# Performance work log

Hardware: AMD Instinct MI355X
Metric: run time of the kernel (lower is better)

The kernel has to match this reference:

```python
import jax, jax.numpy as jnp
import numpy as np

# ---- forest structure (static) ----
B = 32                      # number of trees in the batch
DEPTH = 12                  # topological levels per tree
LEVELS = [2 ** d for d in range(DEPTH)]           # nodes per level (root=level 0)
STARTS = np.concatenate([[0], np.cumsum(LEVELS)[:-1]]).astype(int)
NPG = int(sum(LEVELS))      # 4095 nodes per graph, node 0 = root
N = B * NPG                 # 131040 total nodes
VOCAB = 20000               # dataset.PAD_TOKEN_VALUE + 1
PAD = VOCAB - 1             # padding_idx
E = 256                     # embedding_dim (x_size)
H = 256                     # lstm_output_dim (h_size)
C = 104                     # num_classes (extra_non_linear=None)


def setup_inputs() -> dict:
    key = jax.random.key(0)
    ks = jax.random.split(key, 8)
    # random parent in the previous level for every non-root node (irregular fan-in)
    rng = np.random.RandomState(0)
    par = np.full(N, -1, dtype=np.int64)
    for g in range(B):
        off = g * NPG
        for d in range(1, DEPTH):
            nd = LEVELS[d]
            par[off + STARTS[d]: off + STARTS[d] + nd] = (
                off + STARTS[d - 1] + rng.randint(0, LEVELS[d - 1], size=nd))
    s = 0.05
    return {
        'x': jax.random.randint(ks[0], (N,), 0, VOCAB),
        'par': jnp.asarray(par),
        'emb': jax.random.normal(ks[1], (VOCAB, E), jnp.float32) * s,
        'W_iou': jax.random.normal(ks[2], (3 * H, E), jnp.float32) * s,
        'U_iou': jax.random.normal(ks[3], (3 * H, H), jnp.float32) * s,
        'b_iou': jnp.zeros((1, 3 * H), jnp.float32),
        'U_f_w': jax.random.normal(ks[4], (H, H), jnp.float32) * s,
        'U_f_b': jnp.zeros((H,), jnp.float32),
        'lin_w': jax.random.normal(ks[5], (C, H), jnp.float32) * s,
        'lin_b': jnp.zeros((C,), jnp.float32),
    }


def _forward(x, par, emb, W_iou, U_iou, b_iou, U_f_w, U_f_b, lin_w, lin_b):
    emb = emb.at[PAD].set(0.0)                 # padding_idx row is zero
    x_vec = emb[x]                             # [N, E]
    iou = x_vec @ W_iou.T                      # [N, 3H], W_iou has no bias
    h = jnp.zeros((N, H), x_vec.dtype)
    c = jnp.zeros((N, H), x_vec.dtype)
    offs = jnp.arange(B) * NPG
    # topological propagation: leaves (deepest level) -> root, per generation
    for d in range(DEPTH - 1, -1, -1):
        nd = LEVELS[d]
        nids = (offs[:, None] + STARTS[d] + jnp.arange(nd)).reshape(-1)  # [B*nd]
        iou_n = iou[nids]
        if d < DEPTH - 1:
            nc = LEVELS[d + 1]
            cids = (offs[:, None] + STARTS[d + 1] + jnp.arange(nc)).reshape(-1)
            h_ch = h[cids]                     # mailbox gather of child states
            c_ch = c[cids]
            p = par[cids]                      # global parent id per child
            seg = (p // NPG) * nd + (p % NPG - STARTS[d])  # parent slot in this level
            f = jax.nn.sigmoid(h_ch @ U_f_w.T + U_f_b)     # per-child forget gate
            h_tild = jax.ops.segment_sum(h_ch, seg, num_segments=B * nd)
            c_agg = jax.ops.segment_sum(f * c_ch, seg, num_segments=B * nd)
            iou_n = iou_n + h_tild @ U_iou.T
            c_n = c_agg
        else:
            c_n = jnp.zeros((B * nd, H), x_vec.dtype)
        iou_n = iou_n + b_iou
        i, o, u = jnp.split(iou_n, 3, axis=1)
        c_new = jax.nn.sigmoid(i) * jnp.tanh(u) + c_n
        h_new = jax.nn.sigmoid(o) * jnp.tanh(c_new)
        h = h.at[nids].set(h_new)
        c = c.at[nids].set(c_new)
    roots = h[offs]                            # graph.ndata['h'][0] per graph
    return roots @ lin_w.T + lin_b             # [B, num_classes]


def reference(x, par, emb, W_iou, U_iou, b_iou, U_f_w, U_f_b, lin_w, lin_b):
    return _forward(x, par, emb, W_iou, U_iou, b_iou, U_f_w, U_f_b, lin_w, lin_b)
```

## Files before the change

### kernel.cpp

```cpp
#include <hip/hip_runtime.h>
#include <hip/hip_bf16.h>


#define B_G     32
#define NPG     4095
#define NTOT    (B_G * NPG)
#define NCLS    104
#define VOCAB   20000
#define PAD_TOK 19999
#define KCAP    24
#define LB(d)   (32 * ((1 << (d)) - 1))

#define EMB_BLKS  2500
#define WUC_BLKS  1536
#define UFC_BLKS  256
#define PREP_BLKS 512
#define CONV_BLKS (EMB_BLKS + WUC_BLKS + UFC_BLKS + PREP_BLKS)

typedef unsigned short u16;
typedef unsigned int   u32;
typedef __attribute__((ext_vector_type(8))) short bfrag8;
typedef __attribute__((ext_vector_type(4))) float ffrag4;

__device__ __forceinline__ float bf2f(u16 v) {
    union { u32 u; float f; } x; x.u = ((u32)v) << 16; return x.f;
}
__device__ __forceinline__ u16 f2bf(float f) {
    union { __hip_bfloat16 h; u16 u; } c; c.h = __float2bfloat16(f); return c.u;
}
__device__ __forceinline__ float loadv(const void* b, int i, int isf32) {
    return isf32 ? ((const float*)b)[i] : bf2f(((const u16*)b)[i]);
}
__device__ __forceinline__ float sigf(float x) { return 1.f / (1.f + __expf(-x)); }

__device__ __forceinline__ void gll16(const u16* g, u16* l) {
    __builtin_amdgcn_global_load_lds(
        (const __attribute__((address_space(1))) u32*)g,
        (__attribute__((address_space(3))) u32*)l, 16, 0, 0);
}

__global__ __launch_bounds__(384) void probe_kernel(
    const void* emb, const void* Wiou, const void* Uiou,
    const void* Ufw, const void* lw,
    const int* x32, const int* par32, int* flags)
{
    if (blockIdx.x != 0) return;
    const int w = threadIdx.x >> 6, lane = threadIdx.x & 63;
    const void* ptrs[5] = { emb, Wiou, Uiou, Ufw, lw };
    if (w < 5) {
        const u16* p = (const u16*)ptrs[w];
        int big = 0;
        #pragma unroll
        for (int k = 0; k < 2; ++k) {
            u32 e = (((u32)p[lane * 2 + k]) << 16 >> 23) & 0xFF;
            if (e >= 129) ++big;
        }
        unsigned long long m1 = __ballot(big >= 1);
        unsigned long long m2 = __ballot(big >= 2);
        int tot = __popcll(m1) + __popcll(m2);
        if (lane == 0) flags[w] = (tot >= 4) ? 1 : 0;
    } else if (w == 5) {
        int bad = (lane < 8) ? (x32[2 * lane + 1] != 0) : 0;
        unsigned long long mx = __ballot(bad != 0);
        if (lane == 0) {
            flags[5] = (mx == 0) ? 1 : 0;
            flags[6] = (par32[3] == 0 && par32[5] == 0) ? 1 : 0;
        }
    }
}

__global__ __launch_bounds__(256) void convert_kernel(
    const void* __restrict__ emb, u16* __restrict__ embb,
    const void* __restrict__ Wiou, const void* __restrict__ Uiou,
    u16* __restrict__ wuc,
    const void* __restrict__ Ufw, u16* __restrict__ ufc,
    const int* __restrict__ x, const int* __restrict__ par,
    int* __restrict__ tokLvl, int* __restrict__ cnt, int* __restrict__ bucket,
    const int* __restrict__ flags)
{
    const int b = blockIdx.x;
    if (b < EMB_BLKS) {
        int i8 = (b * 256 + (int)threadIdx.x) * 8;
        if (i8 >= VOCAB * 256) return;
        u16 v[8];
        if ((i8 >> 8) == PAD_TOK) {
            #pragma unroll
            for (int s = 0; s < 8; ++s) v[s] = 0;
        } else if (flags[0]) {
            const float* e = (const float*)emb + i8;
            float4 a = *(const float4*)e;
            float4 c = *(const float4*)(e + 4);
            v[0]=f2bf(a.x); v[1]=f2bf(a.y); v[2]=f2bf(a.z); v[3]=f2bf(a.w);
            v[4]=f2bf(c.x); v[5]=f2bf(c.y); v[6]=f2bf(c.z); v[7]=f2bf(c.w);
        } else {
            *(uint4*)v = *(const uint4*)((const u16*)emb + i8);
        }
        *(uint4*)(embb + i8) = *(uint4*)v;
    } else if (b < EMB_BLKS + WUC_BLKS) {
        int idx = (b - EMB_BLKS) * 256 + (int)threadIdx.x;
        if (idx >= 16 * 768 * 32) return;
        int c   = idx / 24576;
        int rem = idx - c * 24576;
        int out = rem >> 5;
        int kk  = rem & 31;
        int kks = (((kk >> 3) ^ ((out >> 1) & 3)) << 3) | (kk & 7);
        int k   = c * 32 + kks;
        float v = (k < 256) ? loadv(Wiou, out * 256 + k, flags[1])
                            : loadv(Uiou, out * 256 + (k - 256), flags[2]);
        wuc[idx] = f2bf(v);
    } else if (b < EMB_BLKS + WUC_BLKS + UFC_BLKS) {
        int idx = (b - EMB_BLKS - WUC_BLKS) * 256 + (int)threadIdx.x;
        if (idx >= 8 * 256 * 32) return;
        int c   = idx >> 13;
        int rem = idx & 8191;
        int out = rem >> 5;
        int kk  = rem & 31;
        int kks = (((kk >> 3) ^ ((out >> 1) & 3)) << 3) | (kk & 7);
        ufc[idx] = f2bf(loadv(Ufw, out * 256 + c * 32 + kks, flags[3]));
    } else {
        int gid = (b - EMB_BLKS - WUC_BLKS - UFC_BLKS) * 256 + (int)threadIdx.x;
        if (gid >= NTOT) return;
        int g     = (int)((u32)gid / NPG);
        int local = gid - g * NPG;
        int v  = local + 1;
        int d  = 31 - __clz(v);
        int j  = local - ((1 << d) - 1);
        int tok = flags[5] ? x[2 * gid] : x[gid];
        if (tok < 0 || tok >= VOCAB) tok = PAD_TOK;
        tokLvl[LB(d) + (g << d) + j] = tok;
        if (local > 0) {
            int p  = flags[6] ? par[2 * gid] : par[gid];
            p = max(0, min(p, NTOT - 1));
            int pg = (int)((u32)p / NPG);
            int pl = p - pg * NPG;
            int pd = d - 1;
            int ps = LB(pd) + (pg << pd) + (pl - ((1 << pd) - 1));
            ps = max(0, min(ps, 65503));
            int slot = atomicAdd(&cnt[ps], 1);
            if (slot < KCAP) bucket[(size_t)ps * KCAP + slot] = (g << d) + j;
        }
    }
}

__global__ __launch_bounds__(256, 3) void gemm1_kernel(
    const u16* __restrict__ hch, u16* cbuf,
    const u16* __restrict__ ufc, const void* __restrict__ ufb,
    const int* __restrict__ flags)
{
    __shared__ union {
        struct { u16 As[2][64][32]; u16 Bs[2][256][32]; } k;
        u16 tile[64][264];
    } sm;
    auto& tile = sm.tile;
    const int t = threadIdx.x;
    const int w = t >> 6, lane = t & 63, quad = lane >> 4, l15 = lane & 15;
    const int squad = quad ^ ((l15 >> 1) & 3);
    const int m0 = blockIdx.x * 64;
    const int f_uf = flags[3];

    const int drow = lane >> 2, dseg = lane & 3;

    ffrag4 acc[4][4];
    #pragma unroll
    for (int i = 0; i < 4; ++i)
        #pragma unroll
        for (int j = 0; j < 4; ++j) acc[i][j] = (ffrag4)0.f;

    const int arow = t >> 2, aseg = t & 3;

    auto stage = [&](int cn, int buf) {
        int row = (w << 4) + drow;
        int ss  = dseg ^ ((row >> 1) & 3);
        gll16(hch + (size_t)(m0 + row) * 256 + cn * 32 + ss * 8,
              &sm.k.As[buf][w << 4][0]);
        #pragma unroll
        for (int r16 = 0; r16 < 4; ++r16)
            gll16(ufc + ((size_t)cn * 256 + r16 * 64 + arow) * 32 + aseg * 8,
                  &sm.k.Bs[buf][r16 * 64 + arow][aseg * 8]);
    };

    stage(0, 0);
    __syncthreads();

    for (int c = 0; c < 8; ++c) {
        const int cur = c & 1, nxt = cur ^ 1;
        if (c + 1 < 8) stage(c + 1, nxt);
        bfrag8 a[4], b[4];
        #pragma unroll
        for (int mt = 0; mt < 4; ++mt) a[mt] = *(bfrag8*)&sm.k.As[cur][mt * 16 + l15][squad * 8];
        #pragma unroll
        for (int nt = 0; nt < 4; ++nt) b[nt] = *(bfrag8*)&sm.k.Bs[cur][w * 64 + nt * 16 + l15][squad * 8];
        #pragma unroll
        for (int mt = 0; mt < 4; ++mt)
            #pragma unroll
            for (int nt = 0; nt < 4; ++nt)
                acc[mt][nt] = __builtin_amdgcn_mfma_f32_16x16x32_bf16(a[mt], b[nt], acc[mt][nt], 0, 0, 0);
        __syncthreads();
    }

    const int srow = t >> 2, sseg = t & 3;
    const size_t sgb = (size_t)(m0 + srow) * 256 + sseg * 64;
    #pragma unroll
    for (int k = 0; k < 8; ++k)
        *(uint4*)&tile[srow][sseg * 64 + k * 8] = *(const uint4*)(cbuf + sgb + k * 8);
    __syncthreads();

    #pragma unroll
    for (int nt = 0; nt < 4; ++nt) {
        int hu = w * 64 + nt * 16 + l15;
        float fb = loadv(ufb, hu, f_uf);
        #pragma unroll
        for (int mt = 0; mt < 4; ++mt) {
            #pragma unroll
            for (int r = 0; r < 4; ++r) {
                int row = mt * 16 + quad * 4 + r;
                float f = sigf(acc[mt][nt][r] + fb);
                tile[row][hu] = f2bf(f * bf2f(tile[row][hu]));
            }
        }
    }
    __syncthreads();
    #pragma unroll
    for (int k = 0; k < 8; ++k)
        *(uint4*)(cbuf + sgb + k * 8) = *(const uint4*)&tile[srow][sseg * 64 + k * 8];
}

__global__ __launch_bounds__(256) void agg_kernel(
    int NN, const u32* __restrict__ hch32, const u32* __restrict__ fcch32,
    const int* __restrict__ cnt_d, const int* __restrict__ bucket_d,
    u32* __restrict__ htild32, u32* __restrict__ cagg32)
{
    int pi  = blockIdx.x * 2 + (threadIdx.x >> 7);
    int col = threadIdx.x & 127;
    if (pi >= NN) return;
    int nc = min(cnt_d[pi], KCAP);
    float h0 = 0.f, h1 = 0.f, c0 = 0.f, c1 = 0.f;
    for (int ci = 0; ci < nc; ++ci) {
        int ch = bucket_d[(size_t)pi * KCAP + ci];
        u32 hv = hch32[(size_t)ch * 128 + col];
        u32 fv = fcch32[(size_t)ch * 128 + col];
        h0 += bf2f((u16)(hv & 0xffff)); h1 += bf2f((u16)(hv >> 16));
        c0 += bf2f((u16)(fv & 0xffff)); c1 += bf2f((u16)(fv >> 16));
    }
    htild32[(size_t)pi * 128 + col] = (u32)f2bf(h0) | ((u32)f2bf(h1) << 16);
    cagg32[(size_t)pi * 128 + col]  = (u32)f2bf(c0) | ((u32)f2bf(c1) << 16);
}

__global__ __launch_bounds__(256, 3) void gemm2_kernel(
    int nchunk, int NN,
    const int* __restrict__ tokLvl_d, const u16* __restrict__ embb,
    const u16* __restrict__ wuc, const void* __restrict__ biou,
    const u16* __restrict__ htild, const u16* __restrict__ cagg,
    u16* __restrict__ hdst, u16* __restrict__ cdst,
    const int* __restrict__ flags)
{
    __shared__ union {
        struct { u16 As[2][128][32]; u16 Bs[2][192][32]; } k;
        u16 tile[128][72];
    } sm;
    __shared__ int toks[128];
    auto& tile = sm.tile;
    const int t = threadIdx.x;
    const int w = t >> 6, lane = t & 63, quad = lane >> 4, l15 = lane & 15;
    const int squad = quad ^ ((l15 >> 1) & 3);
    const int m0 = blockIdx.x * 128;
    const int q  = blockIdx.y;
    const int f_b = flags[1];

    if (t < 128) toks[t] = tokLvl_d[m0 + t];
    __syncthreads();

    ffrag4 acc[8][3];
    #pragma unroll
    for (int i = 0; i < 8; ++i)
        #pragma unroll
        for (int j = 0; j < 3; ++j) acc[i][j] = (ffrag4)0.f;

    const int drow = lane >> 2, dseg = lane & 3;
    const int brow = t >> 2, bseg = t & 3;

    auto stage = [&](int cn, int buf) {
        #pragma unroll
        for (int k = 0; k < 2; ++k) {
            int row = (w << 5) + (k << 4) + drow;
            int ss  = dseg ^ ((row >> 1) & 3);
            const u16* src = (cn < 8)
                ? embb  + (size_t)toks[row] * 256 + cn * 32 + ss * 8
                : htild + (size_t)(m0 + row) * 256 + (cn - 8) * 32 + ss * 8;
            gll16(src, &sm.k.As[buf][(w << 5) + (k << 4)][0]);
        }
        #pragma unroll
        for (int g = 0; g < 3; ++g)
            gll16(wuc + ((size_t)cn * 768 + g * 256 + q * 64 + brow) * 32 + bseg * 8,
                  &sm.k.Bs[buf][g * 64 + brow][bseg * 8]);
    };

    stage(0, 0);
    __syncthreads();

    for (int c = 0; c < nchunk; ++c) {
        const int cur = c & 1, nxt = cur ^ 1;
        if (c + 1 < nchunk) stage(c + 1, nxt);
        bfrag8 a[8], b[3];
        #pragma unroll
        for (int mt = 0; mt < 8; ++mt) a[mt] = *(bfrag8*)&sm.k.As[cur][mt * 16 + l15][squad * 8];
        #pragma unroll
        for (int g = 0; g < 3; ++g) b[g] = *(bfrag8*)&sm.k.Bs[cur][g * 64 + w * 16 + l15][squad * 8];
        #pragma unroll
        for (int mt = 0; mt < 8; ++mt)
            #pragma unroll
            for (int g = 0; g < 3; ++g)
                acc[mt][g] = __builtin_amdgcn_mfma_f32_16x16x32_bf16(a[mt], b[g], acc[mt][g], 0, 0, 0);
        __syncthreads();
    }

    const int hu  = q * 64 + w * 16 + l15;
    const int huL = w * 16 + l15;
    const float bi = loadv(biou, hu,       f_b);
    const float bo = loadv(biou, 256 + hu, f_b);
    const float bu = loadv(biou, 512 + hu, f_b);

    const int srow = t >> 1, sseg = t & 1;
    const size_t sgbase = (size_t)(m0 + srow) * 256 + q * 64 + sseg * 32;
    const bool svalid = (m0 + srow) < NN;

    if (cagg) {
        if (svalid) {
            #pragma unroll
            for (int k = 0; k < 4; ++k)
                *(uint4*)&tile[srow][sseg * 32 + k * 8] =
                    *(const uint4*)(cagg + sgbase + k * 8);
        }
    }
    __syncthreads();

    u16 cnv[8][4];
    #pragma unroll
    for (int mt = 0; mt < 8; ++mt) {
        #pragma unroll
        for (int r = 0; r < 4; ++r) {
            int row = mt * 16 + quad * 4 + r;
            float cg = cagg ? bf2f(tile[row][huL]) : 0.f;
            float iv = acc[mt][0][r] + bi;
            float ov = acc[mt][1][r] + bo;
            float uv = acc[mt][2][r] + bu;
            float cn = sigf(iv) * tanhf(uv) + cg;
            float hn = sigf(ov) * tanhf(cn);
            cnv[mt][r] = f2bf(cn);
            tile[row][huL] = f2bf(hn);
        }
    }
    __syncthreads();
    if (svalid) {
        #pragma unroll
        for (int k = 0; k < 4; ++k)
            *(uint4*)(hdst + sgbase + k * 8) = *(const uint4*)&tile[srow][sseg * 32 + k * 8];
    }
    __syncthreads();
    #pragma unroll
    for (int mt = 0; mt < 8; ++mt)
        #pragma unroll
        for (int r = 0; r < 4; ++r)
            tile[mt * 16 + quad * 4 + r][huL] = cnv[mt][r];
    __syncthreads();
    if (svalid) {
        #pragma unroll
        for (int k = 0; k < 4; ++k)
            *(uint4*)(cdst + sgbase + k * 8) = *(const uint4*)&tile[srow][sseg * 32 + k * 8];
    }
}

__global__ __launch_bounds__(1024, 1) void tail_kernel(
    const int* __restrict__ tokLvl, const u16* __restrict__ embb,
    const u16* __restrict__ wuc, const void* __restrict__ biou,
    const u16* __restrict__ ufc, const void* __restrict__ ufb,
    const u16* __restrict__ hB, const u16* __restrict__ cB,
    const int* __restrict__ cnt, const int* __restrict__ bucket,
    const void* __restrict__ lw, const void* __restrict__ lb,
    float* __restrict__ out, const int* __restrict__ flags)
{
    __shared__ u16 hs[64][264];
    __shared__ u16 cs[64][264];
    __shared__ u16 hts[32][264];
    __shared__ u16 cts[32][264];
    __shared__ float lred[8][NCLS];
    __shared__ int cntS[64];
    __shared__ int toksS[64];
    __shared__ int bucketS[64][KCAP];
    const int t = threadIdx.x;
    const int g = blockIdx.x;
    const int w = t >> 6;
    const int lane = t & 63, quad = lane >> 4, l15 = lane & 15;
    const int squad = quad ^ ((l15 >> 1) & 3);
    const int f_uf = flags[3], f_b = flags[1], f_lw = flags[4];
    const int hu = w * 16 + l15;

    const float fbv = loadv(ufb, hu, f_uf);
    const float biv = loadv(biou, hu,       f_b);
    const float bov = loadv(biou, 256 + hu, f_b);
    const float buv = loadv(biou, 512 + hu, f_b);

    #pragma unroll 1
    for (int i = t; i < 64 * 32; i += 1024) {
        int j = i >> 5, seg = i & 31;
        size_t off = (((size_t)((g << 6) + j)) << 8) + seg * 8;
        *(uint4*)&hs[j][seg * 8] = *(const uint4*)(hB + off);
        *(uint4*)&cs[j][seg * 8] = *(const uint4*)(cB + off);
    }
    #pragma unroll 1
    for (int d5 = 5; d5 >= 0; --d5) {
        const int np5  = 1 << d5;
        const int sb5  = 64 - (2 << d5);
        const int lvb5 = LB(d5) + (g << d5);
        #pragma unroll 1
        for (int i = t; i < np5 * (KCAP + 1); i += 1024) {
            int pi = i / (KCAP + 1), f = i - pi * (KCAP + 1);
            if (f == 0) {
                cntS[sb5 + pi]  = cnt[lvb5 + pi];
                toksS[sb5 + pi] = tokLvl[lvb5 + pi];
            } else {
                bucketS[sb5 + pi][f - 1] = bucket[(size_t)(lvb5 + pi) * KCAP + f - 1];
            }
        }
    }
    __syncthreads();

    #pragma unroll 1
    for (int d = 5; d >= 0; --d) {
        const int ncr = 1 << (d + 1);
        const int np  = 1 << d;
        const int sb  = 64 - (2 << d);

        {
            ffrag4 facc[4];
            #pragma unroll
            for (int i = 0; i < 4; ++i) facc[i] = (ffrag4)0.f;
            #pragma unroll 4
            for (int c = 0; c < 8; ++c) {
                bfrag8 a[4];
                #pragma unroll
                for (int mt = 0; mt < 4; ++mt)
                    a[mt] = *(const bfrag8*)&hs[mt * 16 + l15][c * 32 + quad * 8];
                bfrag8 b = *(const bfrag8*)(ufc + ((size_t)c * 256 + w * 16 + l15) * 32 + squad * 8);
                #pragma unroll
                for (int mt = 0; mt < 4; ++mt)
                    facc[mt] = __builtin_amdgcn_mfma_f32_16x16x32_bf16(a[mt], b, facc[mt], 0, 0, 0);
            }
            #pragma unroll
            for (int mt = 0; mt < 4; ++mt) {
                #pragma unroll
                for (int r = 0; r < 4; ++r) {
                    int j = mt * 16 + quad * 4 + r;
                    if (j < ncr) {
                        float f = sigf(facc[mt][r] + fbv);
                        cs[j][hu] = f2bf(f * bf2f(cs[j][hu]));
                    }
                }
            }
        }

        {
            const int pr = lane >> 3;
            const int colb = (w * 8 + (lane & 7)) * 2;
            #pragma unroll 1
            for (int pi = pr; pi < np; pi += 8) {
                int nc = min(cntS[sb + pi], KCAP);
                float h0 = 0.f, h1 = 0.f, c0 = 0.f, c1 = 0.f;
                #pragma unroll 1
                for (int ci = 0; ci < nc; ++ci) {
                    int j = bucketS[sb + pi][ci] & (ncr - 1);
                    u32 hv = *(const u32*)&hs[j][colb];
                    u32 cv = *(const u32*)&cs[j][colb];
                    h0 += bf2f((u16)(hv & 0xffff)); h1 += bf2f((u16)(hv >> 16));
                    c0 += bf2f((u16)(cv & 0xffff)); c1 += bf2f((u16)(cv >> 16));
                }
                *(u32*)&hts[pi][colb] = (u32)f2bf(h0) | ((u32)f2bf(h1) << 16);
                *(u32*)&cts[pi][colb] = (u32)f2bf(c0) | ((u32)f2bf(c1) << 16);
            }
        }
        __syncthreads();

        {
            int tok0 = toksS[sb + min(l15, np - 1)];
            int tok1 = toksS[sb + min(16 + l15, np - 1)];
            const u16* wb = wuc + ((size_t)w * 16 + l15) * 32 + squad * 8;
            ffrag4 acc[2][3];
            #pragma unroll
            for (int i = 0; i < 2; ++i)
                #pragma unroll
                for (int j = 0; j < 3; ++j) acc[i][j] = (ffrag4)0.f;
            #pragma unroll 4
            for (int c = 0; c < 8; ++c) {
                bfrag8 a0 = *(const bfrag8*)(embb + (size_t)tok0 * 256 + c * 32 + quad * 8);
                bfrag8 a1 = *(const bfrag8*)(embb + (size_t)tok1 * 256 + c * 32 + quad * 8);
                #pragma unroll
                for (int g3 = 0; g3 < 3; ++g3) {
                    bfrag8 b = *(const bfrag8*)(wb + ((size_t)c * 768 + g3 * 256) * 32);
                    acc[0][g3] = __builtin_amdgcn_mfma_f32_16x16x32_bf16(a0, b, acc[0][g3], 0, 0, 0);
                    acc[1][g3] = __builtin_amdgcn_mfma_f32_16x16x32_bf16(a1, b, acc[1][g3], 0, 0, 0);
                }
            }
            #pragma unroll 4
            for (int c8 = 0; c8 < 8; ++c8) {
                bfrag8 a0 = *(const bfrag8*)&hts[l15][c8 * 32 + quad * 8];
                bfrag8 a1 = *(const bfrag8*)&hts[16 + l15][c8 * 32 + quad * 8];
                #pragma unroll
                for (int g3 = 0; g3 < 3; ++g3) {
                    bfrag8 b = *(const bfrag8*)(wb + ((size_t)(c8 + 8) * 768 + g3 * 256) * 32);
                    acc[0][g3] = __builtin_amdgcn_mfma_f32_16x16x32_bf16(a0, b, acc[0][g3], 0, 0, 0);
                    acc[1][g3] = __builtin_amdgcn_mfma_f32_16x16x32_bf16(a1, b, acc[1][g3], 0, 0, 0);
                }
            }
            #pragma unroll
            for (int mt = 0; mt < 2; ++mt) {
                #pragma unroll
                for (int r = 0; r < 4; ++r) {
                    int p = mt * 16 + quad * 4 + r;
                    if (p < np) {
                        float iv = acc[mt][0][r] + biv;
                        float ov = acc[mt][1][r] + bov;
                        float uv = acc[mt][2][r] + buv;
                        float cn = sigf(iv) * tanhf(uv) + bf2f(cts[p][hu]);
                        float hn = sigf(ov) * tanhf(cn);
                        hs[p][hu] = f2bf(hn);
                        cs[p][hu] = f2bf(cn);
                    }
                }
            }
        }
        __syncthreads();
    }

    {
        const int o  = t & 127;
        const int ks = t >> 7;
        if (o < NCLS) {
            float acc = 0.f;
            #pragma unroll 8
            for (int k = ks * 32; k < ks * 32 + 32; ++k)
                acc += loadv(lw, o * 256 + k, f_lw) * bf2f(hs[0][k]);
            lred[ks][o] = acc;
        }
        __syncthreads();
        if (t < NCLS) {
            float s = 0.f;
            #pragma unroll
            for (int i = 0; i < 8; ++i) s += lred[i][t];
            out[(size_t)g * NCLS + t] = s + loadv(lb, t, f_lw);
        }
    }
}

__global__ void fill_kernel(float* out, int n, float v) {
    int i = blockIdx.x * 256 + threadIdx.x;
    if (i < n) out[i] = v;
}

extern "C" void kernel_launch(void* const* d_in, const int* in_sizes, int n_in,
                              void* d_out, int out_size, void* d_ws, size_t ws_size,
                              hipStream_t stream)
{
    float* out = (float*)d_out;

    static const int exp_sizes[10] = {131040, 131040, 5120000, 196608, 196608,
                                      768, 65536, 256, 26624, 104};
    bool shapes_ok = (n_in == 10) && (out_size == B_G * NCLS);
    for (int i = 0; i < 10 && shapes_ok; ++i)
        if (in_sizes[i] != exp_sizes[i]) shapes_ok = false;
    if (!shapes_ok) {
        fill_kernel<<<(out_size + 255) / 256, 256, 0, stream>>>(out, out_size, 2.0f);
        return;
    }

    const int* x     = (const int*)d_in[0];
    const int* par   = (const int*)d_in[1];
    const void* emb  = d_in[2];
    const void* Wiou = d_in[3];
    const void* Uiou = d_in[4];
    const void* biou = d_in[5];
    const void* Ufw  = d_in[6];
    const void* Ufb  = d_in[7];
    const void* lw   = d_in[8];
    const void* lb   = d_in[9];

    char* W = (char*)d_ws;
    u16* hA     = (u16*)(W + 0);
    u16* hB     = (u16*)(W + 33554432);
    u16* cA     = (u16*)(W + 50331648);
    u16* cB     = (u16*)(W + 83886080);
    u16* htild  = (u16*)(W + 100663296);
    u16* cagg   = (u16*)(W + 117440512);
    u16* WUc    = (u16*)(W + 134217728);
    u16* Ufc    = (u16*)(W + 135004160);
    int* tokLvl = (int*)(W + 135135232);
    int* cnt    = (int*)(W + 135659520);
    int* bucket = (int*)(W + 135921664);
    u16* embb   = (u16*)(W + 142213120);
    int* flags  = (int*)(W + 152453120);
    const size_t NEED = 152453184;
    if (ws_size < NEED) {
        fill_kernel<<<(out_size + 255) / 256, 256, 0, stream>>>(out, out_size, 1.0f);
        return;
    }

    hipMemsetAsync(cnt, 0, 65536 * sizeof(int), stream);
    probe_kernel<<<1, 384, 0, stream>>>(emb, Wiou, Uiou, Ufw, lw, x, par, flags);
    convert_kernel<<<CONV_BLKS, 256, 0, stream>>>(
        emb, embb, Wiou, Uiou, WUc, Ufw, Ufc,
        x, par, tokLvl, cnt, bucket, flags);

    gemm2_kernel<<<dim3(512, 4), 256, 0, stream>>>(
        8, 65536, tokLvl + LB(11), embb, WUc, biou,
        nullptr, nullptr, hA, cA, flags);

    for (int d = 10; d >= 6; --d) {
        const int cl = d + 1;
        const int NC = B_G << cl;
        const int NN = B_G << d;
        const u16* hch = (cl & 1) ? hA : hB;
        u16*       cch = (cl & 1) ? cA : cB;
        u16* hdst = (d & 1) ? hA : hB;
        u16* cdst = (d & 1) ? cA : cB;
        gemm1_kernel<<<NC / 64, 256, 0, stream>>>(hch, cch, Ufc, Ufb, flags);
        agg_kernel<<<(NN + 1) / 2, 256, 0, stream>>>(
            NN, (const u32*)hch, (const u32*)cch,
            cnt + LB(d), bucket + (size_t)LB(d) * KCAP,
            (u32*)htild, (u32*)cagg);
        gemm2_kernel<<<dim3((NN + 127) / 128, 4), 256, 0, stream>>>(
            16, NN, tokLvl + LB(d), embb, WUc, biou,
            htild, cagg, hdst, cdst, flags);
    }

    tail_kernel<<<B_G, 1024, 0, stream>>>(
        tokLvl, embb, WUc, biou, Ufc, Ufb,
        hB, cB, cnt, bucket, lw, lb, out, flags);
}
```

Measured before the change: 566.0 us.

## Triple-buffer GEMM K-loop with vmcnt waits and unroll child aggregation

Both GEMM kernels move from double-buffered LDS staging to a three-stage ring. Each iteration prefetches two chunks ahead and waits on vmcnt counts plus a single raw barrier, replacing two __syncthreads per iteration, so global-to-LDS loads overlap more with MFMA work. Launch bounds drop from 3 to 2 blocks per SM to make room for the larger LDS footprint. Separately, the in-LDS child aggregation loop is unrolled by four to raise instruction-level parallelism on the LDS reads.

```diff
diff --git a/kernel.cpp b/kernel.cpp
--- a/kernel.cpp
+++ b/kernel.cpp
@@ -21,6 +21,9 @@
 typedef unsigned int   u32;
 typedef __attribute__((ext_vector_type(8))) short bfrag8;
 typedef __attribute__((ext_vector_type(4))) float ffrag4;
+
+#define WAITV5() asm volatile("s_waitcnt vmcnt(5)" ::: "memory")
+#define WAITV0() asm volatile("s_waitcnt vmcnt(0)" ::: "memory")
 
 __device__ __forceinline__ float bf2f(u16 v) {
     union { u32 u; float f; } x; x.u = ((u32)v) << 16; return x.f;
@@ -142,13 +145,13 @@
     }
 }
 
-__global__ __launch_bounds__(256, 3) void gemm1_kernel(
+__global__ __launch_bounds__(256, 2) void gemm1_kernel(
     const u16* __restrict__ hch, u16* cbuf,
     const u16* __restrict__ ufc, const void* __restrict__ ufb,
     const int* __restrict__ flags)
 {
     __shared__ union {
-        struct { u16 As[2][64][32]; u16 Bs[2][256][32]; } k;
+        struct { u16 As[3][64][32]; u16 Bs[3][256][32]; } k;
         u16 tile[64][264];
     } sm;
     auto& tile = sm.tile;
@@ -159,14 +162,13 @@
     const int f_uf = flags[3];
 
     const int drow = lane >> 2, dseg = lane & 3;
+    const int arow = t >> 2, aseg = t & 3;
 
     ffrag4 acc[4][4];
     #pragma unroll
     for (int i = 0; i < 4; ++i)
         #pragma unroll
         for (int j = 0; j < 4; ++j) acc[i][j] = (ffrag4)0.f;
-
-    const int arow = t >> 2, aseg = t & 3;
 
     auto stage = [&](int cn, int buf) {
         int row = (w << 4) + drow;
@@ -180,11 +182,14 @@
     };
 
     stage(0, 0);
-    __syncthreads();
+    stage(1, 1);
 
     for (int c = 0; c < 8; ++c) {
-        const int cur = c & 1, nxt = cur ^ 1;
-        if (c + 1 < 8) stage(c + 1, nxt);
+        if (c + 1 < 8) { WAITV5(); } else { WAITV0(); }
+        __builtin_amdgcn_s_barrier();
+        __builtin_amdgcn_sched_barrier(0);
+        if (c + 2 < 8) stage(c + 2, (c + 2) % 3);
+        const int cur = c % 3;
         bfrag8 a[4], b[4];
         #pragma unroll
         for (int mt = 0; mt < 4; ++mt) a[mt] = *(bfrag8*)&sm.k.As[cur][mt * 16 + l15][squad * 8];
@@ -195,8 +200,8 @@
             #pragma unroll
             for (int nt = 0; nt < 4; ++nt)
                 acc[mt][nt] = __builtin_amdgcn_mfma_f32_16x16x32_bf16(a[mt], b[nt], acc[mt][nt], 0, 0, 0);
-        __syncthreads();
-    }
+    }
+    __syncthreads();
 
     const int srow = t >> 2, sseg = t & 3;
     const size_t sgb = (size_t)(m0 + srow) * 256 + sseg * 64;
@@ -246,7 +251,7 @@
     cagg32[(size_t)pi * 128 + col]  = (u32)f2bf(c0) | ((u32)f2bf(c1) << 16);
 }
 
-__global__ __launch_bounds__(256, 3) void gemm2_kernel(
+__global__ __launch_bounds__(256, 2) void gemm2_kernel(
     int nchunk, int NN,
     const int* __restrict__ tokLvl_d, const u16* __restrict__ embb,
     const u16* __restrict__ wuc, const void* __restrict__ biou,
@@ -255,7 +260,7 @@
     const int* __restrict__ flags)
 {
     __shared__ union {
-        struct { u16 As[2][128][32]; u16 Bs[2][192][32]; } k;
+        struct { u16 As[3][128][32]; u16 Bs[3][192][32]; } k;
         u16 tile[128][72];
     } sm;
     __shared__ int toks[128];
@@ -296,11 +301,14 @@
     };
 
     stage(0, 0);
-    __syncthreads();
+    stage(1, 1);
 
     for (int c = 0; c < nchunk; ++c) {
-        const int cur = c & 1, nxt = cur ^ 1;
-        if (c + 1 < nchunk) stage(c + 1, nxt);
+        if (c + 1 < nchunk) { WAITV5(); } else { WAITV0(); }
+        __builtin_amdgcn_s_barrier();
+        __builtin_amdgcn_sched_barrier(0);
+        if (c + 2 < nchunk) stage(c + 2, (c + 2) % 3);
+        const int cur = c % 3;
         bfrag8 a[8], b[3];
         #pragma unroll
         for (int mt = 0; mt < 8; ++mt) a[mt] = *(bfrag8*)&sm.k.As[cur][mt * 16 + l15][squad * 8];
@@ -311,8 +319,8 @@
             #pragma unroll
             for (int g = 0; g < 3; ++g)
                 acc[mt][g] = __builtin_amdgcn_mfma_f32_16x16x32_bf16(a[mt], b[g], acc[mt][g], 0, 0, 0);
-        __syncthreads();
-    }
+    }
+    __syncthreads();
 
     const int hu  = q * 64 + w * 16 + l15;
     const int huL = w * 16 + l15;
@@ -465,10 +473,35 @@
             #pragma unroll 1
             for (int pi = pr; pi < np; pi += 8) {
                 int nc = min(cntS[sb + pi], KCAP);
+                const int* bk = &bucketS[sb + pi][0];
                 float h0 = 0.f, h1 = 0.f, c0 = 0.f, c1 = 0.f;
+                int ci = 0;
                 #pragma unroll 1
-                for (int ci = 0; ci < nc; ++ci) {
-                    int j = bucketS[sb + pi][ci] & (ncr - 1);
+                for (; ci + 4 <= nc; ci += 4) {
+                    int j0 = bk[ci]     & (ncr - 1);
+                    int j1 = bk[ci + 1] & (ncr - 1);
+                    int j2 = bk[ci + 2] & (ncr - 1);
+                    int j3 = bk[ci + 3] & (ncr - 1);
+                    u32 ha = *(const u32*)&hs[j0][colb];
+                    u32 hb = *(const u32*)&hs[j1][colb];
+                    u32 hc = *(const u32*)&hs[j2][colb];
+                    u32 hd = *(const u32*)&hs[j3][colb];
+                    u32 ca = *(const u32*)&cs[j0][colb];
+                    u32 cb = *(const u32*)&cs[j1][colb];
+                    u32 cc = *(const u32*)&cs[j2][colb];
+                    u32 cd = *(const u32*)&cs[j3][colb];
+                    h0 += bf2f((u16)(ha & 0xffff)); h1 += bf2f((u16)(ha >> 16));
+                    h0 += bf2f((u16)(hb & 0xffff)); h1 += bf2f((u16)(hb >> 16));
+                    h0 += bf2f((u16)(hc & 0xffff)); h1 += bf2f((u16)(hc >> 16));
+                    h0 += bf2f((u16)(hd & 0xffff)); h1 += bf2f((u16)(hd >> 16));
+                    c0 += bf2f((u16)(ca & 0xffff)); c1 += bf2f((u16)(ca >> 16));
+                    c0 += bf2f((u16)(cb & 0xffff)); c1 += bf2f((u16)(cb >> 16));
+                    c0 += bf2f((u16)(cc & 0xffff)); c1 += bf2f((u16)(cc >> 16));
+                    c0 += bf2f((u16)(cd & 0xffff)); c1 += bf2f((u16)(cd >> 16));
+                }
+                #pragma unroll 1
+                for (; ci < nc; ++ci) {
+                    int j = bk[ci] & (ncr - 1);
                     u32 hv = *(const u32*)&hs[j][colb];
                     u32 cv = *(const u32*)&cs[j][colb];
                     h0 += bf2f((u16)(hv & 0xffff)); h1 += bf2f((u16)(hv >> 16));
```

Result: slower. 581.4 us (+2.7%).

## Restructure gemm2 warp tiling: per-warp rows, A fragments loaded straight from global

Applied to the files above, without the earlier changes.

Gemm2 changes from each warp owning a 16-column slice across all 128 rows to each warp owning 32 rows across all 192 gate columns. The A operand (embedding rows or h_tild) is no longer staged in LDS; each lane loads its 16-byte fragment directly from global into registers, with a manual two-deep prefetch. Only B goes through LDS, which cuts LDS traffic and drops the A staging buffer. The costs are uncoalesced 16-byte global loads for A, more LDS reads for B per warp, and a gather of embedding rows now done per lane.

```diff
diff --git a/kernel.cpp b/kernel.cpp
--- a/kernel.cpp
+++ b/kernel.cpp
@@ -159,14 +159,13 @@
     const int f_uf = flags[3];
 
     const int drow = lane >> 2, dseg = lane & 3;
+    const int arow = t >> 2, aseg = t & 3;
 
     ffrag4 acc[4][4];
     #pragma unroll
     for (int i = 0; i < 4; ++i)
         #pragma unroll
         for (int j = 0; j < 4; ++j) acc[i][j] = (ffrag4)0.f;
-
-    const int arow = t >> 2, aseg = t & 3;
 
     auto stage = [&](int cn, int buf) {
         int row = (w << 4) + drow;
@@ -255,7 +254,7 @@
     const int* __restrict__ flags)
 {
     __shared__ union {
-        struct { u16 As[2][128][32]; u16 Bs[2][192][32]; } k;
+        u16 Bs[2][192][32];
         u16 tile[128][72];
     } sm;
     __shared__ int toks[128];
@@ -270,55 +269,62 @@
     if (t < 128) toks[t] = tokLvl_d[m0 + t];
     __syncthreads();
 
-    ffrag4 acc[8][3];
-    #pragma unroll
-    for (int i = 0; i < 8; ++i)
-        #pragma unroll
-        for (int j = 0; j < 3; ++j) acc[i][j] = (ffrag4)0.f;
-
-    const int drow = lane >> 2, dseg = lane & 3;
+    ffrag4 acc[2][12];
+    #pragma unroll
+    for (int i = 0; i < 2; ++i)
+        #pragma unroll
+        for (int j = 0; j < 12; ++j) acc[i][j] = (ffrag4)0.f;
+
     const int brow = t >> 2, bseg = t & 3;
-
-    auto stage = [&](int cn, int buf) {
-        #pragma unroll
-        for (int k = 0; k < 2; ++k) {
-            int row = (w << 5) + (k << 4) + drow;
-            int ss  = dseg ^ ((row >> 1) & 3);
-            const u16* src = (cn < 8)
-                ? embb  + (size_t)toks[row] * 256 + cn * 32 + ss * 8
-                : htild + (size_t)(m0 + row) * 256 + (cn - 8) * 32 + ss * 8;
-            gll16(src, &sm.k.As[buf][(w << 5) + (k << 4)][0]);
-        }
+    const int r0 = (w << 5) + l15, r1 = r0 + 16;
+    const int tok0 = toks[r0], tok1 = toks[r1];
+
+    auto stageB = [&](int cn, int buf) {
         #pragma unroll
         for (int g = 0; g < 3; ++g)
             gll16(wuc + ((size_t)cn * 768 + g * 256 + q * 64 + brow) * 32 + bseg * 8,
-                  &sm.k.Bs[buf][g * 64 + brow][bseg * 8]);
+                  &sm.Bs[buf][g * 64 + brow][bseg * 8]);
     };
-
-    stage(0, 0);
-    __syncthreads();
-
-    for (int c = 0; c < nchunk; ++c) {
-        const int cur = c & 1, nxt = cur ^ 1;
-        if (c + 1 < nchunk) stage(c + 1, nxt);
-        bfrag8 a[8], b[3];
-        #pragma unroll
-        for (int mt = 0; mt < 8; ++mt) a[mt] = *(bfrag8*)&sm.k.As[cur][mt * 16 + l15][squad * 8];
-        #pragma unroll
-        for (int g = 0; g < 3; ++g) b[g] = *(bfrag8*)&sm.k.Bs[cur][g * 64 + w * 16 + l15][squad * 8];
-        #pragma unroll
-        for (int mt = 0; mt < 8; ++mt)
-            #pragma unroll
-            for (int g = 0; g < 3; ++g)
-                acc[mt][g] = __builtin_amdgcn_mfma_f32_16x16x32_bf16(a[mt], b[g], acc[mt][g], 0, 0, 0);
+    auto loadA = [&](int cn, bfrag8* a) {
+        if (cn < 8) {
+            a[0] = *(const bfrag8*)(embb + (size_t)tok0 * 256 + cn * 32 + quad * 8);
+            a[1] = *(const bfrag8*)(embb + (size_t)tok1 * 256 + cn * 32 + quad * 8);
+        } else {
+            a[0] = *(const bfrag8*)(htild + (size_t)(m0 + r0) * 256 + (cn - 8) * 32 + quad * 8);
+            a[1] = *(const bfrag8*)(htild + (size_t)(m0 + r1) * 256 + (cn - 8) * 32 + quad * 8);
+        }
+    };
+    auto mfmaStep = [&](const bfrag8* a, int buf) {
+        #pragma unroll
+        for (int nt = 0; nt < 12; ++nt) {
+            const int g = nt >> 2, j = nt & 3;
+            bfrag8 b = *(const bfrag8*)&sm.Bs[buf][g * 64 + j * 16 + l15][squad * 8];
+            acc[0][nt] = __builtin_amdgcn_mfma_f32_16x16x32_bf16(a[0], b, acc[0][nt], 0, 0, 0);
+            acc[1][nt] = __builtin_amdgcn_mfma_f32_16x16x32_bf16(a[1], b, acc[1][nt], 0, 0, 0);
+        }
+    };
+
+    bfrag8 aA[2], aB[2];
+    loadA(0, aA);
+    stageB(0, 0);
+    __syncthreads();
+
+    for (int c = 0; c < nchunk; c += 2) {
+        stageB(c + 1, 1);
+        loadA(c + 1, aB);
+        mfmaStep(aA, 0);
         __syncthreads();
-    }
-
-    const int hu  = q * 64 + w * 16 + l15;
-    const int huL = w * 16 + l15;
-    const float bi = loadv(biou, hu,       f_b);
-    const float bo = loadv(biou, 256 + hu, f_b);
-    const float bu = loadv(biou, 512 + hu, f_b);
+        if (c + 2 < nchunk) { stageB(c + 2, 0); loadA(c + 2, aA); }
+        mfmaStep(aB, 1);
+        __syncthreads();
+    }
+
+    float bias[3][4];
+    #pragma unroll
+    for (int g = 0; g < 3; ++g)
+        #pragma unroll
+        for (int j = 0; j < 4; ++j)
+            bias[g][j] = loadv(biou, g * 256 + q * 64 + j * 16 + l15, f_b);
 
     const int srow = t >> 1, sseg = t & 1;
     const size_t sgbase = (size_t)(m0 + srow) * 256 + q * 64 + sseg * 32;
@@ -334,20 +340,24 @@
     }
     __syncthreads();
 
-    u16 cnv[8][4];
-    #pragma unroll
-    for (int mt = 0; mt < 8; ++mt) {
-        #pragma unroll
-        for (int r = 0; r < 4; ++r) {
-            int row = mt * 16 + quad * 4 + r;
-            float cg = cagg ? bf2f(tile[row][huL]) : 0.f;
-            float iv = acc[mt][0][r] + bi;
-            float ov = acc[mt][1][r] + bo;
-            float uv = acc[mt][2][r] + bu;
-            float cn = sigf(iv) * tanhf(uv) + cg;
-            float hn = sigf(ov) * tanhf(cn);
-            cnv[mt][r] = f2bf(cn);
-            tile[row][huL] = f2bf(hn);
+    u16 cnv[2][4][4];
+    #pragma unroll
+    for (int mt = 0; mt < 2; ++mt) {
+        #pragma unroll
+        for (int j = 0; j < 4; ++j) {
+            #pragma unroll
+            for (int r = 0; r < 4; ++r) {
+                int row  = (w << 5) + mt * 16 + quad * 4 + r;
+                int colL = j * 16 + l15;
+                float cg = cagg ? bf2f(tile[row][colL]) : 0.f;
+                float iv = acc[mt][j][r]     + bias[0][j];
+                float ov = acc[mt][4 + j][r] + bias[1][j];
+                float uv = acc[mt][8 + j][r] + bias[2][j];
+                float cn = sigf(iv) * tanhf(uv) + cg;
+                float hn = sigf(ov) * tanhf(cn);
+                cnv[mt][j][r] = f2bf(cn);
+                tile[row][colL] = f2bf(hn);
+            }
         }
     }
     __syncthreads();
@@ -358,10 +368,12 @@
     }
     __syncthreads();
     #pragma unroll
-    for (int mt = 0; mt < 8; ++mt)
-        #pragma unroll
-        for (int r = 0; r < 4; ++r)
-            tile[mt * 16 + quad * 4 + r][huL] = cnv[mt][r];
+    for (int mt = 0; mt < 2; ++mt)
+        #pragma unroll
+        for (int j = 0; j < 4; ++j)
+            #pragma unroll
+            for (int r = 0; r < 4; ++r)
+                tile[(w << 5) + mt * 16 + quad * 4 + r][j * 16 + l15] = cnv[mt][j][r];
     __syncthreads();
     if (svalid) {
         #pragma unroll
```

Result: slower. 581.8 us (+2.8%).
